# Kernel optimization log

Measured on AMD Instinct MI355X. Metric: run time of the kernel, lower is better.

The kernel has to match this reference:

```python
import jax, jax.numpy as jnp
import numpy as np

N_EMBD = 1024
N_HEAD = 16
B, T = 4, 2048


def setup_inputs() -> dict:
    key = jax.random.key(0)
    k1, k2, k3, k4, k5 = jax.random.split(key, 5)
    s = 0.02
    return {
        "x": jax.random.normal(k1, (B, T, N_EMBD), dtype=jnp.float32),
        "w_attn": jax.random.normal(k2, (N_EMBD, 3 * N_EMBD), dtype=jnp.float32) * s,
        "b_attn": jnp.zeros((3 * N_EMBD,), dtype=jnp.float32),
        "w_proj": jax.random.normal(k3, (N_EMBD, N_EMBD), dtype=jnp.float32) * s,
        "b_proj": jnp.zeros((N_EMBD,), dtype=jnp.float32),
    }


def reference(x, w_attn, b_attn, w_proj, b_proj):
    Bb, Tt, C = x.shape
    hd = C // N_HEAD  # head dim
    qkv = x @ w_attn + b_attn                      # [B,T,3C]
    q, k, v = jnp.split(qkv, 3, axis=-1)
    # [B,T,C] -> [B,H,T,hd]
    def heads(t):
        return t.reshape(Bb, Tt, N_HEAD, hd).transpose(0, 2, 1, 3)
    q, k, v = heads(q), heads(k), heads(v)
    scale = 1.0 / np.sqrt(hd).astype(np.float32)
    attn = jnp.einsum("bhqd,bhkd->bhqk", q, k) * scale  # [B,H,T,T]
    causal = jnp.tril(jnp.ones((Tt, Tt), dtype=bool))
    attn = jnp.where(causal, attn, -jnp.inf)
    attn = jax.nn.softmax(attn, axis=-1)
    y = jnp.einsum("bhqk,bhkd->bhqd", attn, v)          # [B,H,T,hd]
    y = y.transpose(0, 2, 1, 3).reshape(Bb, Tt, C)
    return y @ w_proj + b_proj
```

## Files before the change

### kernel.cpp

```cpp
#include <hip/hip_runtime.h>
#include <cmath>


typedef short short8 __attribute__((ext_vector_type(8)));
typedef short short4v __attribute__((ext_vector_type(4)));
typedef float f32x4 __attribute__((ext_vector_type(4)));

__device__ __forceinline__ short f2bf(float f) {
  unsigned u = __builtin_bit_cast(unsigned, f);
  u = (u + 0x7fffu + ((u >> 16) & 1u)) >> 16;
  return (short)u;
}

__device__ __forceinline__ float exp2_fast(float x) {
  float r;
  asm("v_exp_f32 %0, %1" : "=v"(r) : "v"(x));
  return r;
}

__device__ __forceinline__ void gld_lds16(const void* g, void* l) {
  __builtin_amdgcn_global_load_lds(
      (__attribute__((address_space(1))) void*)g,
      (__attribute__((address_space(3))) void*)l,
      16, 0, 0);
}

__device__ __forceinline__ void barx() {
  asm volatile("s_barrier" ::: "memory");
}

template <int IMM>
__device__ __forceinline__ short8 dsr(int addr) {
  short8 d;
  asm volatile("ds_read_b128 %0, %1 offset:%2"
               : "=v"(d) : "v"(addr), "n"(IMM));
  return d;
}

#define WAITL()                                       \
  asm volatile("s_waitcnt lgkmcnt(0)" ::: "memory");  \
  __builtin_amdgcn_sched_barrier(0);

__global__ void cast_bf16_kernel(const float* __restrict__ in,
                                 short* __restrict__ out, int n4) {
  int i = blockIdx.x * blockDim.x + threadIdx.x;
  if (i < n4) {
    const float4 v = ((const float4*)in)[i];
    short4v o;
    o.x = f2bf(v.x); o.y = f2bf(v.y); o.z = f2bf(v.z); o.w = f2bf(v.w);
    ((short4v*)out)[i] = o;
  }
}

__global__ void transpose_cast_kernel(const float* __restrict__ in,
                                      short* __restrict__ out, int R, int C) {
  __shared__ float tile[32][33];
  int c0 = blockIdx.x * 32, r0 = blockIdx.y * 32;
  int tx = threadIdx.x & 31, tg = threadIdx.x >> 5;
#pragma unroll
  for (int i = 0; i < 4; ++i) {
    int r = tg * 4 + i;
    tile[r][tx] = in[(size_t)(r0 + r) * C + c0 + tx];
  }
  __syncthreads();
#pragma unroll
  for (int i = 0; i < 4; ++i) {
    int c = tg * 4 + i;
    out[(size_t)(c0 + c) * R + r0 + tx] = f2bf(tile[tx][c]);
  }
}


#define DOMFMA(mp)                                                           \
  __builtin_amdgcn_s_setprio(1);                                             \
  _Pragma("unroll") for (int i_ = 0; i_ < 2; ++i_)                           \
  _Pragma("unroll") for (int n_ = 0; n_ < 4; ++n_)                           \
  _Pragma("unroll") for (int kh_ = 0; kh_ < 2; ++kh_)                        \
      acc[(mp) + i_][n_] = __builtin_amdgcn_mfma_f32_16x16x32_bf16(          \
          a[i_][kh_], b[n_][kh_], acc[(mp) + i_][n_], 0, 0, 0);              \
  __builtin_amdgcn_s_setprio(0);

__global__ __launch_bounds__(512, 2) void qkv_gemm_kernel(
    const short* __restrict__ A, const short* __restrict__ Bt,
    const float* __restrict__ bias,
    short* __restrict__ oq, short* __restrict__ ok, short* __restrict__ ovt,
    int M, int N, int K) {
  extern __shared__ short lds[];
  const int NT = K >> 6;
  const int lane = threadIdx.x & 63, wave = threadIdx.x >> 6;
  const int quad = lane >> 4, l16 = lane & 15;
  const int wm2 = wave >> 2, wn4 = wave & 3;

  const int nbn = N >> 8;
  const int swz = (blockIdx.x & 7) * ((int)gridDim.x >> 3) + (blockIdx.x >> 3);
  const int m0 = (swz / nbn) * 256, n0 = (swz % nbn) * 256;

  const int r8 = lane >> 3;
  const int sw8 = ((lane & 7) ^ r8) * 8;
  const short* Ab0 = A + (size_t)(m0 + wave * 8 + r8) * K + sw8;
  const short* Bb0 = Bt + (size_t)(n0 + wave * 8 + r8) * K + sw8;
  short* ldsw = lds + wave * 512;

  auto stage = [&](int t, int mat, int rA, int rB) {
    const short* g = (mat ? Bb0 : Ab0) + t * 64;
    short* d = ldsw + (t & 1) * 32768 + mat * 16384;
    gld_lds16(g + (size_t)rA * K, d + rA * 64);
    gld_lds16(g + (size_t)rB * K, d + rB * 64);
  };

  const int swz0 = ((0 + quad) ^ (l16 & 7)) * 16;
  const int swz1 = ((4 + quad) ^ (l16 & 7)) * 16;
  const int baseA0 = wm2 * 16384 + l16 * 128 + swz0;
  const int baseA1 = wm2 * 16384 + l16 * 128 + swz1;
  const int baseB0 = 32768 + wn4 * 8192 + l16 * 128 + swz0;
  const int baseB1 = 32768 + wn4 * 8192 + l16 * 128 + swz1;

  f32x4 acc[8][4] = {};

  stage(0, 1, 0, 64);
  stage(0, 1, 128, 192);
  stage(0, 0, 0, 128);
  stage(0, 0, 64, 192);
  stage(1, 1, 0, 64);
  stage(1, 1, 128, 192);
  stage(1, 0, 0, 128);
  asm volatile("s_waitcnt vmcnt(6)" ::: "memory");
  barx();

#pragma unroll 1
  for (int t = 0; t < NT; ++t) {
    const int vb = (t & 1) << 16;
    const int aA0 = baseA0 + vb, aA1 = baseA1 + vb;
    const int aB0 = baseB0 + vb, aB1 = baseB1 + vb;
    short8 b[4][2], a[2][2];

    b[0][0] = dsr<0>(aB0);      b[0][1] = dsr<0>(aB1);
    b[1][0] = dsr<2048>(aB0);   b[1][1] = dsr<2048>(aB1);
    b[2][0] = dsr<4096>(aB0);   b[2][1] = dsr<4096>(aB1);
    b[3][0] = dsr<6144>(aB0);   b[3][1] = dsr<6144>(aB1);
    a[0][0] = dsr<0>(aA0);      a[0][1] = dsr<0>(aA1);
    a[1][0] = dsr<2048>(aA0);   a[1][1] = dsr<2048>(aA1);
    if (t + 1 < NT) stage(t + 1, 0, 64, 192);
    barx();
    WAITL()
    DOMFMA(0)
    barx();

    a[0][0] = dsr<4096>(aA0);   a[0][1] = dsr<4096>(aA1);
    a[1][0] = dsr<6144>(aA0);   a[1][1] = dsr<6144>(aA1);
    if (t + 2 < NT) stage(t + 2, 1, 0, 64);
    barx();
    WAITL()
    DOMFMA(2)
    barx();

    a[0][0] = dsr<8192>(aA0);   a[0][1] = dsr<8192>(aA1);
    a[1][0] = dsr<10240>(aA0);  a[1][1] = dsr<10240>(aA1);
    if (t + 2 < NT) stage(t + 2, 1, 128, 192);
    barx();
    WAITL()
    DOMFMA(4)
    barx();

    a[0][0] = dsr<12288>(aA0);  a[0][1] = dsr<12288>(aA1);
    a[1][0] = dsr<14336>(aA0);  a[1][1] = dsr<14336>(aA1);
    if (t + 2 < NT) stage(t + 2, 0, 0, 128);
    barx();
    WAITL()
    DOMFMA(6)
    if (t == NT - 2)
      asm volatile("s_waitcnt vmcnt(0)" ::: "memory");
    else
      asm volatile("s_waitcnt vmcnt(6)" ::: "memory");
    barx();
  }

  const int sec = n0 >> 10;
  const int h0 = (n0 & 1023) >> 6;
  const float scale = (sec == 0) ? 0.18033688f : 1.0f;
  float bv[4];
#pragma unroll
  for (int n_ = 0; n_ < 4; ++n_) bv[n_] = bias[n0 + wn4 * 64 + n_ * 16 + l16];
  const int b_ = m0 >> 11, t0 = m0 & 2047;

  if (sec < 2) {
    short* dst = (sec == 0) ? oq : ok;
#pragma unroll 1
    for (int p = 0; p < 2; ++p) {
      if (wm2 == p) {
#pragma unroll
        for (int mt = 0; mt < 8; ++mt)
#pragma unroll
          for (int n_ = 0; n_ < 4; ++n_) {
            const int col = wn4 * 64 + n_ * 16 + l16;
#pragma unroll
            for (int r = 0; r < 4; ++r)
              lds[(mt * 16 + quad * 4 + r) * 264 + col] =
                  f2bf((acc[mt][n_][r] + bv[n_]) * scale);
          }
      }
      __syncthreads();
      const int hl = wave & 3, rg = wave >> 2;
      const short* sp = &lds[(rg * 64 + r8) * 264 + hl * 64 + (lane & 7) * 8];
      short* gp = dst +
          ((size_t)(b_ * 16 + h0 + hl) * 2048 + t0 + p * 128 + rg * 64 + r8) * 64 +
          (lane & 7) * 8;
#pragma unroll
      for (int i = 0; i < 8; ++i)
        *(short8*)(gp + (size_t)i * 512) = *(const short8*)(sp + i * 8 * 264);
      __syncthreads();
    }
  } else {
#pragma unroll 1
    for (int p = 0; p < 2; ++p) {
      if (wm2 == p) {
#pragma unroll
        for (int mt = 0; mt < 8; ++mt)
#pragma unroll
          for (int n_ = 0; n_ < 4; ++n_) {
            const int col = wn4 * 64 + n_ * 16 + l16;
#pragma unroll
            for (int r = 0; r < 4; ++r)
              lds[col * 136 + mt * 16 + quad * 4 + r] =
                  f2bf(acc[mt][n_][r] + bv[n_]);
          }
      }
      __syncthreads();
      const int cw = wave * 32 + (lane >> 4);
#pragma unroll
      for (int i = 0; i < 8; ++i) {
        const int c = cw + i * 4;
        const int bh = b_ * 16 + h0 + (c >> 6), d = c & 63;
        *(short8*)(ovt + ((size_t)bh * 64 + d) * 2048 + t0 + p * 128 +
                   (lane & 15) * 8) =
            *(const short8*)&lds[c * 136 + (lane & 15) * 8];
      }
      __syncthreads();
    }
  }
}

template <int MODE>
__global__ __launch_bounds__(256) void gemm_bt_kernel(
    const short* __restrict__ A, const short* __restrict__ Bt,
    const float* __restrict__ bias, float* __restrict__ outf,
    short* __restrict__ oq, short* __restrict__ ok, short* __restrict__ ovt,
    int M, int N, int K) {
  __shared__ short slds[16384];
  short* As = slds;
  short* Bs = slds + 8192;
  const int m0 = blockIdx.y * 128, n0 = blockIdx.x * 128;
  const int lane = threadIdx.x & 63, wave = threadIdx.x >> 6;
  const int quad = lane >> 4, l16 = lane & 15;
  const int wm = (wave >> 1) * 64, wn = (wave & 1) * 64;

  const int row_off = lane >> 3;
  const int segsw = ((lane & 7) ^ row_off) * 8;
  const short* Ag = A + (size_t)(m0 + wave * 32 + row_off) * K + segsw;
  const short* Bg = Bt + (size_t)(n0 + wave * 32 + row_off) * K + segsw;

  f32x4 acc[4][4] = {};

  for (int k0 = 0; k0 < K; k0 += 64) {
#pragma unroll
    for (int g = 0; g < 4; ++g) {
      gld_lds16(Ag + (size_t)(g * 8) * K + k0, &As[(wave * 32 + g * 8) * 64]);
      gld_lds16(Bg + (size_t)(g * 8) * K + k0, &Bs[(wave * 32 + g * 8) * 64]);
    }
    __syncthreads();
#pragma unroll
    for (int kh = 0; kh < 2; ++kh) {
      short8 a[4], b[4];
#pragma unroll
      for (int t = 0; t < 4; ++t) {
        const int R = wm + t * 16 + l16;
        a[t] = *(const short8*)&As[R * 64 + (((kh * 4 + quad) ^ (R & 7)) * 8)];
      }
#pragma unroll
      for (int t = 0; t < 4; ++t) {
        const int R = wn + t * 16 + l16;
        b[t] = *(const short8*)&Bs[R * 64 + (((kh * 4 + quad) ^ (R & 7)) * 8)];
      }
#pragma unroll
      for (int mt = 0; mt < 4; ++mt)
#pragma unroll
        for (int nt = 0; nt < 4; ++nt)
          acc[mt][nt] = __builtin_amdgcn_mfma_f32_16x16x32_bf16(
              a[mt], b[nt], acc[mt][nt], 0, 0, 0);
    }
    __syncthreads();
  }

  float bv[4];
#pragma unroll
  for (int nt = 0; nt < 4; ++nt) bv[nt] = bias[n0 + wn + nt * 16 + l16];

  if (MODE == 1) {
#pragma unroll
    for (int mt = 0; mt < 4; ++mt)
#pragma unroll
      for (int nt = 0; nt < 4; ++nt) {
        const int n = n0 + wn + nt * 16 + l16;
#pragma unroll
        for (int r = 0; r < 4; ++r) {
          const int m = m0 + wm + mt * 16 + quad * 4 + r;
          outf[(size_t)m * N + n] = acc[mt][nt][r] + bv[nt];
        }
      }
  }
}

__global__ __launch_bounds__(256, 6) void attn_kernel(
    const short* __restrict__ q, const short* __restrict__ k,
    const short* __restrict__ vt, short* __restrict__ y) {
  __shared__ short Ks[64 * 64];
  __shared__ short Vs[64 * 64];
  __shared__ short Ps[4][16 * 72];
  const int lane = threadIdx.x & 63, wave = threadIdx.x >> 6;
  const int quad = lane >> 4, l16 = lane & 15;
  const int g = blockIdx.x;
  const int bh = g & 63;
  const int j = 31 - (g >> 6);
  const int b_ = bh >> 4, h = bh & 15;
  const int q0 = j * 64 + wave * 16;

  const short* qbh = q + (size_t)bh * 2048 * 64;
  const short* kbh = k + (size_t)bh * 2048 * 64;
  const short* vbh = vt + (size_t)bh * 64 * 2048;
  short* Pw = Ps[wave];

  const short8 qf0 = *(const short8*)&qbh[(q0 + l16) * 64 + quad * 8];
  const short8 qf1 = *(const short8*)&qbh[(q0 + l16) * 64 + 32 + quad * 8];

  short8 ones;
#pragma unroll
  for (int i = 0; i < 8; ++i) ones[i] = (short)0x3F80;

  f32x4 O[4] = {};
  f32x4 lacc = {};

  const int srow = lane >> 3;
  const int scol = ((lane & 7) ^ srow) * 8;
  const int r0s = wave * 16;

#pragma unroll 1
  for (int c = 0; c <= j; ++c) {
    const int kt0 = c * 64;
    gld_lds16(kbh + (size_t)(kt0 + r0s + srow) * 64 + scol, &Ks[r0s * 64]);
    gld_lds16(kbh + (size_t)(kt0 + r0s + 8 + srow) * 64 + scol, &Ks[(r0s + 8) * 64]);
    gld_lds16(vbh + (size_t)(r0s + srow) * 2048 + kt0 + scol, &Vs[r0s * 64]);
    gld_lds16(vbh + (size_t)(r0s + 8 + srow) * 2048 + kt0 + scol, &Vs[(r0s + 8) * 64]);
    __syncthreads();

    const int sw = l16 & 7;
    f32x4 sc4[4];
#pragma unroll
    for (int cf = 0; cf < 4; ++cf) {
      const int row = cf * 16 + l16;
      const short8 kfa = *(const short8*)&Ks[row * 64 + ((quad ^ sw) * 8)];
      const short8 kfb = *(const short8*)&Ks[row * 64 + (((quad + 4) ^ sw) * 8)];
      f32x4 z = {};
      z = __builtin_amdgcn_mfma_f32_16x16x32_bf16(qf0, kfa, z, 0, 0, 0);
      z = __builtin_amdgcn_mfma_f32_16x16x32_bf16(qf1, kfb, z, 0, 0, 0);
      sc4[cf] = z;
    }

    if (c == j) {
#pragma unroll
      for (int cf = 0; cf < 4; ++cf) {
        const int col = kt0 + cf * 16 + l16;
#pragma unroll
        for (int r = 0; r < 4; ++r) {
          const int rowg = q0 + quad * 4 + r;
          float e = exp2_fast(sc4[cf][r]);
          e = (col > rowg) ? 0.f : e;
          Pw[(quad * 4 + r) * 72 + cf * 16 + l16] = f2bf(e);
        }
      }
    } else {
#pragma unroll
      for (int cf = 0; cf < 4; ++cf)
#pragma unroll
        for (int r = 0; r < 4; ++r)
          Pw[(quad * 4 + r) * 72 + cf * 16 + l16] = f2bf(exp2_fast(sc4[cf][r]));
    }
    asm volatile("s_waitcnt lgkmcnt(0)" ::: "memory");
    const short8 pf0 = *(const short8*)&Pw[l16 * 72 + quad * 8];
    const short8 pf1 = *(const short8*)&Pw[l16 * 72 + 32 + quad * 8];

    lacc = __builtin_amdgcn_mfma_f32_16x16x32_bf16(pf0, ones, lacc, 0, 0, 0);
    lacc = __builtin_amdgcn_mfma_f32_16x16x32_bf16(pf1, ones, lacc, 0, 0, 0);

#pragma unroll
    for (int dt = 0; dt < 4; ++dt) {
      const int d = dt * 16 + l16;
      const short8 vf0 = *(const short8*)&Vs[d * 64 + ((quad ^ sw) * 8)];
      const short8 vf1 = *(const short8*)&Vs[d * 64 + (((quad + 4) ^ sw) * 8)];
      O[dt] = __builtin_amdgcn_mfma_f32_16x16x32_bf16(pf0, vf0, O[dt], 0, 0, 0);
      O[dt] = __builtin_amdgcn_mfma_f32_16x16x32_bf16(pf1, vf1, O[dt], 0, 0, 0);
    }
    __syncthreads();
  }

  float inv[4];
#pragma unroll
  for (int r = 0; r < 4; ++r) inv[r] = 1.0f / lacc[r];
#pragma unroll
  for (int dt = 0; dt < 4; ++dt) {
    const int d = dt * 16 + l16;
#pragma unroll
    for (int r = 0; r < 4; ++r) {
      const int t_ = q0 + quad * 4 + r;
      y[((size_t)b_ * 2048 + t_) * 1024 + h * 64 + d] = f2bf(O[dt][r] * inv[r]);
    }
  }
}

extern "C" void kernel_launch(void* const* d_in, const int* in_sizes, int n_in,
                              void* d_out, int out_size, void* d_ws, size_t ws_size,
                              hipStream_t stream) {
  const float* x      = (const float*)d_in[0];
  const float* w_attn = (const float*)d_in[1];
  const float* b_attn = (const float*)d_in[2];
  const float* w_proj = (const float*)d_in[3];
  const float* b_proj = (const float*)d_in[4];
  float* out = (float*)d_out;

  short* xb  = (short*)d_ws;
  short* wTa = xb + (size_t)8192 * 1024;
  short* wTp = wTa + (size_t)3072 * 1024;
  short* qb  = wTp + (size_t)1024 * 1024;
  short* kb  = qb + (size_t)64 * 2048 * 64;
  short* vtb = kb + (size_t)64 * 2048 * 64;
  short* yb  = vtb + (size_t)64 * 2048 * 64;

  static int lds_attr_done = 0;
  if (!lds_attr_done) {
    (void)hipFuncSetAttribute(reinterpret_cast<const void*>(qkv_gemm_kernel),
                              hipFuncAttributeMaxDynamicSharedMemorySize,
                              131072);
    lds_attr_done = 1;
  }

  cast_bf16_kernel<<<8192, 256, 0, stream>>>(x, xb, 8192 * 1024 / 4);
  transpose_cast_kernel<<<dim3(96, 32), 256, 0, stream>>>(w_attn, wTa, 1024, 3072);
  transpose_cast_kernel<<<dim3(32, 32), 256, 0, stream>>>(w_proj, wTp, 1024, 1024);

  qkv_gemm_kernel<<<384, 512, 131072, stream>>>(
      xb, wTa, b_attn, qb, kb, vtb, 8192, 3072, 1024);

  attn_kernel<<<2048, 256, 0, stream>>>(qb, kb, vtb, yb);

  gemm_bt_kernel<1><<<dim3(8, 64), 256, 0, stream>>>(
      yb, wTp, b_proj, out, nullptr, nullptr, nullptr, 8192, 1024, 1024);
}
```

Baseline: 250.6 us.

## Simplify QKV GEMM pipeline to single-stage prefetch with two MFMA phases per tile

Replaces the four-phase, staggered two-tile-ahead load schedule in the QKV GEMM main loop with a simpler scheme. Each K-tile now issues every global-to-LDS stage for the next tile at once, then runs two MFMA phases, one per k-half, each loading all A and B fragments. Intermediate barriers are removed, leaving one wait for all loads and one barrier per tile. This cuts barrier count and scheduling complexity, but prefetch depth drops to one tile and more fragments are held in registers at once.

```diff
diff --git a/kernel.cpp b/kernel.cpp
--- a/kernel.cpp
+++ b/kernel.cpp
@@ -70,15 +70,6 @@
   }
 }
 
-
-#define DOMFMA(mp)                                                           \
-  __builtin_amdgcn_s_setprio(1);                                             \
-  _Pragma("unroll") for (int i_ = 0; i_ < 2; ++i_)                           \
-  _Pragma("unroll") for (int n_ = 0; n_ < 4; ++n_)                           \
-  _Pragma("unroll") for (int kh_ = 0; kh_ < 2; ++kh_)                        \
-      acc[(mp) + i_][n_] = __builtin_amdgcn_mfma_f32_16x16x32_bf16(          \
-          a[i_][kh_], b[n_][kh_], acc[(mp) + i_][n_], 0, 0, 0);              \
-  __builtin_amdgcn_s_setprio(0);
 
 __global__ __launch_bounds__(512, 2) void qkv_gemm_kernel(
     const short* __restrict__ A, const short* __restrict__ Bt,
@@ -121,10 +112,7 @@
   stage(0, 1, 128, 192);
   stage(0, 0, 0, 128);
   stage(0, 0, 64, 192);
-  stage(1, 1, 0, 64);
-  stage(1, 1, 128, 192);
-  stage(1, 0, 0, 128);
-  asm volatile("s_waitcnt vmcnt(6)" ::: "memory");
+  asm volatile("s_waitcnt vmcnt(0)" ::: "memory");
   barx();
 
 #pragma unroll 1
@@ -132,46 +120,48 @@
     const int vb = (t & 1) << 16;
     const int aA0 = baseA0 + vb, aA1 = baseA1 + vb;
     const int aB0 = baseB0 + vb, aB1 = baseB1 + vb;
-    short8 b[4][2], a[2][2];
-
-    b[0][0] = dsr<0>(aB0);      b[0][1] = dsr<0>(aB1);
-    b[1][0] = dsr<2048>(aB0);   b[1][1] = dsr<2048>(aB1);
-    b[2][0] = dsr<4096>(aB0);   b[2][1] = dsr<4096>(aB1);
-    b[3][0] = dsr<6144>(aB0);   b[3][1] = dsr<6144>(aB1);
-    a[0][0] = dsr<0>(aA0);      a[0][1] = dsr<0>(aA1);
-    a[1][0] = dsr<2048>(aA0);   a[1][1] = dsr<2048>(aA1);
-    if (t + 1 < NT) stage(t + 1, 0, 64, 192);
-    barx();
+    short8 a[8], b[4];
+
+    b[0] = dsr<0>(aB0);     b[1] = dsr<2048>(aB0);
+    b[2] = dsr<4096>(aB0);  b[3] = dsr<6144>(aB0);
+    a[0] = dsr<0>(aA0);     a[1] = dsr<2048>(aA0);
+    a[2] = dsr<4096>(aA0);  a[3] = dsr<6144>(aA0);
+    a[4] = dsr<8192>(aA0);  a[5] = dsr<10240>(aA0);
+    a[6] = dsr<12288>(aA0); a[7] = dsr<14336>(aA0);
+    if (t + 1 < NT) {
+      stage(t + 1, 1, 0, 64);
+      stage(t + 1, 1, 128, 192);
+      stage(t + 1, 0, 0, 128);
+      stage(t + 1, 0, 64, 192);
+    }
     WAITL()
-    DOMFMA(0)
-    barx();
-
-    a[0][0] = dsr<4096>(aA0);   a[0][1] = dsr<4096>(aA1);
-    a[1][0] = dsr<6144>(aA0);   a[1][1] = dsr<6144>(aA1);
-    if (t + 2 < NT) stage(t + 2, 1, 0, 64);
-    barx();
+    __builtin_amdgcn_s_setprio(1);
+#pragma unroll
+    for (int i_ = 0; i_ < 8; ++i_)
+#pragma unroll
+      for (int n_ = 0; n_ < 4; ++n_)
+        acc[i_][n_] = __builtin_amdgcn_mfma_f32_16x16x32_bf16(
+            a[i_], b[n_], acc[i_][n_], 0, 0, 0);
+    __builtin_amdgcn_s_setprio(0);
+
+    b[0] = dsr<0>(aB1);     b[1] = dsr<2048>(aB1);
+    b[2] = dsr<4096>(aB1);  b[3] = dsr<6144>(aB1);
+    a[0] = dsr<0>(aA1);     a[1] = dsr<2048>(aA1);
+    a[2] = dsr<4096>(aA1);  a[3] = dsr<6144>(aA1);
+    a[4] = dsr<8192>(aA1);  a[5] = dsr<10240>(aA1);
+    a[6] = dsr<12288>(aA1); a[7] = dsr<14336>(aA1);
     WAITL()
-    DOMFMA(2)
-    barx();
-
-    a[0][0] = dsr<8192>(aA0);   a[0][1] = dsr<8192>(aA1);
-    a[1][0] = dsr<10240>(aA0);  a[1][1] = dsr<10240>(aA1);
-    if (t + 2 < NT) stage(t + 2, 1, 128, 192);
-    barx();
-    WAITL()
-    DOMFMA(4)
-    barx();
-
-    a[0][0] = dsr<12288>(aA0);  a[0][1] = dsr<12288>(aA1);
-    a[1][0] = dsr<14336>(aA0);  a[1][1] = dsr<14336>(aA1);
-    if (t + 2 < NT) stage(t + 2, 0, 0, 128);
-    barx();
-    WAITL()
-    DOMFMA(6)
-    if (t == NT - 2)
+    __builtin_amdgcn_s_setprio(1);
+#pragma unroll
+    for (int i_ = 0; i_ < 8; ++i_)
+#pragma unroll
+      for (int n_ = 0; n_ < 4; ++n_)
+        acc[i_][n_] = __builtin_amdgcn_mfma_f32_16x16x32_bf16(
+            a[i_], b[n_], acc[i_][n_], 0, 0, 0);
+    __builtin_amdgcn_s_setprio(0);
+
+    if (t + 1 < NT)
       asm volatile("s_waitcnt vmcnt(0)" ::: "memory");
-    else
-      asm volatile("s_waitcnt vmcnt(6)" ::: "memory");
     barx();
   }
 
```

After: 244.7 us. -2.4%, faster.
